# Kernel tuning notes

Measured on AMD Instinct MI355X. Metric: run time of the kernel, lower is better.

The kernel has to match this reference:

```python
import jax, jax.numpy as jnp
import numpy as np

N = 131072      # total nodes
B = 512         # number of graphs
F_DIM = 512     # in_channels
H = F_DIM // 2  # score_net hidden
RATIO = 0.5
MARGIN = 0.5
TOPK_LOSS_WEIGHT = 0.2


def setup_inputs() -> dict:
    key = jax.random.key(0)
    k1, k2, k3 = jax.random.split(key, 3)
    x = jax.random.normal(k1, (N, F_DIM), dtype=jnp.float32)
    # sorted segment ids: equal-sized graphs of N // B nodes
    batch = (jnp.arange(N) // (N // B)).astype(jnp.int32)
    W1 = jax.random.normal(k2, (F_DIM, H), dtype=jnp.float32) / np.sqrt(F_DIM).astype(np.float32)
    b1 = jnp.zeros((H,), dtype=jnp.float32)
    W2 = jax.random.normal(k3, (H, 1), dtype=jnp.float32) / np.sqrt(H).astype(np.float32)
    b2 = jnp.zeros((1,), dtype=jnp.float32)
    return {"x": x, "batch": batch, "W1": W1, "b1": b1, "W2": W2, "b2": b2}


def reference(x, batch, W1, b1, W2, b2):
    # scores = score_net(x).squeeze(-1)   [N]
    scores = (jax.nn.relu(x @ W1 + b1) @ W2 + b2)[:, 0]

    # per-graph node counts and k = max(1, int(ratio * n_i))
    counts = jax.ops.segment_sum(jnp.ones((N,), dtype=scores.dtype), batch, num_segments=B)
    k = jnp.maximum(1, jnp.floor(RATIO * counts).astype(jnp.int32))  # [B]

    # segmented top-k via lexsort: sort by (batch asc, score desc)
    order = jnp.lexsort((-scores, batch))          # [N] permutation
    b_sorted = batch[order]
    starts = jnp.cumsum(counts) - counts           # exclusive-cumsum segment starts
    rank = jnp.arange(N, dtype=counts.dtype) - starts[b_sorted]  # rank within graph (0 = highest score)
    sel_sorted = rank < k[b_sorted].astype(counts.dtype)
    selected_mask = jnp.zeros((N,), dtype=bool).at[order].set(sel_sorted)

    # global_add_pool over selected nodes
    m = selected_mask.astype(x.dtype)
    x_pooled = jax.ops.segment_sum(x * m[:, None], batch, num_segments=B)  # [B, F]

    # margin regularization loss per graph
    sel_cnt = jax.ops.segment_sum(m, batch, num_segments=B)
    sel_sum = jax.ops.segment_sum(scores * m, batch, num_segments=B)
    tot_sum = jax.ops.segment_sum(scores, batch, num_segments=B)
    uns_cnt = counts - sel_cnt
    sel_mean = sel_sum / jnp.maximum(sel_cnt, 1.0)
    uns_mean = (tot_sum - sel_sum) / jnp.maximum(uns_cnt, 1.0)
    per_graph = jnp.where(uns_cnt > 0, jax.nn.relu(MARGIN - (sel_mean - uns_mean)), 0.0)
    topk_loss = per_graph.sum() / B * TOPK_LOSS_WEIGHT

    return x_pooled, topk_loss, selected_mask
```

## Files before the change

kernel.cpp:

```cpp
#include <hip/hip_runtime.h>

#define BGRAPHS 512
#define FDIM    512
#define HDIM    256
#define NPG     256
#define KSEL    128
#define STAGES  32
#define BSTAGE_SHORTS 8192
#define BSTG    16384
#define A_ROW   24
#define A_PLANE (128 * A_ROW)

typedef __attribute__((ext_vector_type(8)))  _Float16 f16x8;
typedef __attribute__((ext_vector_type(8)))  short    s16x8;
typedef __attribute__((ext_vector_type(16))) float    f32x16;

__device__ __forceinline__ unsigned short f16_rne(float f, float* back) {
    _Float16 h = (_Float16)f;
    *back = (float)h;
    union { _Float16 h; unsigned short s; } cv; cv.h = h;
    return cv.s;
}

__global__ __launch_bounds__(256)
void split_w1_kernel(const float* __restrict__ W1, unsigned short* __restrict__ wsB,
                     float* __restrict__ out_loss)
{
    if (blockIdx.x == 0 && threadIdx.x == 0) out_loss[0] = 0.f;

    const int uid  = blockIdx.x * 256 + threadIdx.x;
    const int lane = uid & 63;
    int t = uid >> 6;
    const int nt = t & 7;  t >>= 3;
    const int p  = t & 1;  t >>= 1;
    const int s  = t;
    const int n  = nt * 32 + (lane & 31);
    const int k0 = s * 16 + (lane >> 5) * 8;

    s16x8 v;
    #pragma unroll
    for (int j = 0; j < 8; ++j) {
        float w = W1[(size_t)(k0 + j) * HDIM + n] * 1024.0f;
        float f1, f2;
        unsigned short h1 = f16_rne(w, &f1);
        unsigned short h2 = f16_rne(w - f1, &f2);
        v[j] = (short)(p ? h2 : h1);
    }
    *(s16x8*)(wsB + (size_t)uid * 8) = v;
}

__global__ __launch_bounds__(512, 4)
void gemm_kernel(const float* __restrict__ x,
                 const unsigned short* __restrict__ wsB,
                 const float* __restrict__ b1, const float* __restrict__ W2,
                 const float* __restrict__ b2,
                 float* __restrict__ scores_out)
{
    __shared__ __attribute__((aligned(16))) unsigned char smem[73728];

    const int bid  = blockIdx.x;
    const int g    = bid >> 1;
    const int rh   = bid & 1;
    const int tid  = threadIdx.x;
    const int lane = tid & 63;
    const int wv   = tid >> 6;
    const int wy   = wv & 1;
    const int wx   = wv >> 1;
    const int l31  = lane & 31;
    const int lh   = lane >> 5;

    const int arow  = tid >> 2;
    const int achk  = tid & 3;
    const float* aptr = x + ((size_t)(g * NPG + rh * 128 + arow)) * FDIM + achk * 4;

    f32x16 acc[2][2];
    #pragma unroll
    for (int a = 0; a < 2; ++a)
        #pragma unroll
        for (int b = 0; b < 2; ++b)
            #pragma unroll
            for (int rr = 0; rr < 16; ++rr) acc[a][b][rr] = 0.f;

    float4 pfA, pfB;

#define GLL_B(OFF, S1) do {                                                     \
    const unsigned short* _src = wsB + (size_t)(S1) * BSTAGE_SHORTS;            \
    unsigned short* _dst = (unsigned short*)(smem + (OFF));                     \
    _Pragma("unroll")                                                           \
    for (int _i = 0; _i < 2; ++_i) {                                            \
        const int _u = _i * 512 + tid;                                          \
        __builtin_amdgcn_global_load_lds(                                       \
            (const __attribute__((address_space(1))) unsigned int*)(_src + (size_t)_u * 8), \
            (__attribute__((address_space(3))) unsigned int*)(_dst + _u * 8),   \
            16, 0, 0);                                                          \
    } } while (0)

#define LOAD_PF(P,S2) do { P = *(const float4*)(aptr + (S2) * 16); } while (0)

#define CONVERT_A(P,BUF) do {                                                   \
    float _f[4] = {P.x, P.y, P.z, P.w};                                         \
    unsigned short _H[4], _M[4];                                                \
    _Pragma("unroll")                                                           \
    for (int _j = 0; _j < 4; ++_j) {                                            \
        float _b1v, _b2v;                                                       \
        float _xs = _f[_j] * 64.0f;                            \
        _H[_j] = f16_rne(_xs, &_b1v);                                           \
        _M[_j] = f16_rne(_xs - _b1v, &_b2v);                                    \
        (void)_b2v;                                                             \
    }                                                                           \
    unsigned short* _pl = (unsigned short*)(smem + 49152 + (BUF) * 12288)       \
                          + arow * A_ROW + achk * 4;                            \
    uint2 _uH, _uM;                                                             \
    _uH.x = (unsigned)_H[0] | ((unsigned)_H[1] << 16);                          \
    _uH.y = (unsigned)_H[2] | ((unsigned)_H[3] << 16);                          \
    _uM.x = (unsigned)_M[0] | ((unsigned)_M[1] << 16);                          \
    _uM.y = (unsigned)_M[2] | ((unsigned)_M[3] << 16);                          \
    *(uint2*)_pl = _uH;                                                         \
    *(uint2*)(_pl + A_PLANE) = _uM;                                             \
    } while (0)

#define COMPUTE(OFFB, ABUF) do {                                                \
    const f16x8* _bfp = (const f16x8*)(smem + (OFFB));                          \
    const unsigned short* _aB = (const unsigned short*)(smem + 49152 + (ABUF) * 12288); \
    const int _a0 = (wy * 64 + l31) * A_ROW + lh * 8;                           \
    f16x8 A0h = *(const f16x8*)(_aB + _a0);                                     \
    f16x8 A0m = *(const f16x8*)(_aB + A_PLANE + _a0);                           \
    f16x8 A1h = *(const f16x8*)(_aB + _a0 + 32 * A_ROW);                        \
    f16x8 A1m = *(const f16x8*)(_aB + A_PLANE + _a0 + 32 * A_ROW);              \
    const int _nn = wx * 2;                                                     \
    f16x8 Bh0 = _bfp[(0 * 8 + _nn + 0) * 64 + lane];                            \
    f16x8 Bh1 = _bfp[(0 * 8 + _nn + 1) * 64 + lane];                            \
    f16x8 Bm0 = _bfp[(1 * 8 + _nn + 0) * 64 + lane];                            \
    f16x8 Bm1 = _bfp[(1 * 8 + _nn + 1) * 64 + lane];                            \
    __builtin_amdgcn_s_setprio(1);                                              \
    acc[0][0] = __builtin_amdgcn_mfma_f32_32x32x16_f16(A0h, Bh0, acc[0][0], 0, 0, 0); \
    acc[0][1] = __builtin_amdgcn_mfma_f32_32x32x16_f16(A0h, Bh1, acc[0][1], 0, 0, 0); \
    acc[1][0] = __builtin_amdgcn_mfma_f32_32x32x16_f16(A1h, Bh0, acc[1][0], 0, 0, 0); \
    acc[1][1] = __builtin_amdgcn_mfma_f32_32x32x16_f16(A1h, Bh1, acc[1][1], 0, 0, 0); \
    acc[0][0] = __builtin_amdgcn_mfma_f32_32x32x16_f16(A0m, Bh0, acc[0][0], 0, 0, 0); \
    acc[0][1] = __builtin_amdgcn_mfma_f32_32x32x16_f16(A0m, Bh1, acc[0][1], 0, 0, 0); \
    acc[1][0] = __builtin_amdgcn_mfma_f32_32x32x16_f16(A1m, Bh0, acc[1][0], 0, 0, 0); \
    acc[1][1] = __builtin_amdgcn_mfma_f32_32x32x16_f16(A1m, Bh1, acc[1][1], 0, 0, 0); \
    acc[0][0] = __builtin_amdgcn_mfma_f32_32x32x16_f16(A0h, Bm0, acc[0][0], 0, 0, 0); \
    acc[0][1] = __builtin_amdgcn_mfma_f32_32x32x16_f16(A0h, Bm1, acc[0][1], 0, 0, 0); \
    acc[1][0] = __builtin_amdgcn_mfma_f32_32x32x16_f16(A1h, Bm0, acc[1][0], 0, 0, 0); \
    acc[1][1] = __builtin_amdgcn_mfma_f32_32x32x16_f16(A1h, Bm1, acc[1][1], 0, 0, 0); \
    __builtin_amdgcn_s_setprio(0);                                              \
    } while (0)

#define SYNC3 do {                                                              \
    asm volatile("s_waitcnt vmcnt(3) lgkmcnt(0)" ::: "memory");                 \
    __builtin_amdgcn_s_barrier();                                               \
    __builtin_amdgcn_sched_barrier(0); } while (0)
#define SYNC0 do {                                                              \
    asm volatile("s_waitcnt vmcnt(0) lgkmcnt(0)" ::: "memory");                 \
    __builtin_amdgcn_s_barrier();                                               \
    __builtin_amdgcn_sched_barrier(0); } while (0)

    LOAD_PF(pfA, 0);  GLL_B(0, 0);
    LOAD_PF(pfB, 1);  GLL_B(BSTG, 1);
    CONVERT_A(pfA, 0);
    SYNC3;

    int o0 = 0, o1 = BSTG, o2 = 2 * BSTG;
    for (int s = 0; s < 30; s += 2) {
        LOAD_PF(pfA, s + 2);  GLL_B(o2, s + 2);
        COMPUTE(o0, 0);
        CONVERT_A(pfB, 1);
        SYNC3;

        LOAD_PF(pfB, s + 3);  GLL_B(o0, s + 3);
        COMPUTE(o1, 1);
        CONVERT_A(pfA, 0);
        SYNC3;

        const int t = o0; o0 = o2; o2 = o1; o1 = t;
    }

    COMPUTE(o0, 0);
    CONVERT_A(pfB, 1);
    SYNC0;
    COMPUTE(o1, 1);

    float* scr = (float*)smem;

    float bb[2], ww[2];
    #pragma unroll
    for (int nt = 0; nt < 2; ++nt) {
        const int cc = wx * 64 + nt * 32 + l31;
        bb[nt] = b1[cc];
        ww[nt] = W2[cc];
    }
    const float unscale = 1.0f / 65536.0f;
    #pragma unroll
    for (int mt = 0; mt < 2; ++mt) {
        float pr[16];
        #pragma unroll
        for (int rr = 0; rr < 16; ++rr) pr[rr] = 0.f;
        #pragma unroll
        for (int nt = 0; nt < 2; ++nt)
            #pragma unroll
            for (int rr = 0; rr < 16; ++rr) {
                float h = fmaf(acc[mt][nt][rr], unscale, bb[nt]);
                h = h > 0.f ? h : 0.f;
                pr[rr] = fmaf(h, ww[nt], pr[rr]);
            }
        #pragma unroll
        for (int mask = 1; mask <= 16; mask <<= 1)
            #pragma unroll
            for (int rr = 0; rr < 16; ++rr)
                pr[rr] += __shfl_xor(pr[rr], mask);
        if (l31 == 0) {
            #pragma unroll
            for (int rr = 0; rr < 16; ++rr) {
                const int row = wy * 64 + mt * 32 + (rr & 3) + 8 * (rr >> 2) + 4 * lh;
                scr[wx * 128 + row] = pr[rr];
            }
        }
    }
    __syncthreads();

    if (tid < 128) {
        const float s = b2[0] + scr[tid] + scr[128 + tid] + scr[256 + tid] + scr[384 + tid];
        scores_out[(size_t)g * FDIM + rh * 128 + tid] = s;
    }

#undef GLL_B
#undef LOAD_PF
#undef CONVERT_A
#undef COMPUTE
#undef SYNC3
#undef SYNC0
}

__global__ __launch_bounds__(512)
void select_pool_kernel(const float* __restrict__ x,
                        float* __restrict__ pooled,
                        float* __restrict__ mask_out,
                        float* __restrict__ out_loss)
{
    __shared__ float sv[NPG];
    __shared__ int   selr[KSEL];
    __shared__ float redT[NPG];
    __shared__ float redS[NPG];

    const int g   = blockIdx.x;
    const int tid = threadIdx.x;

    float sc = 0.f;
    if (tid < NPG) {
        sc = pooled[(size_t)g * FDIM + tid];
        sv[tid] = sc;
    }
    __syncthreads();

    if (tid < NPG) {
        int rank = 0;
        for (int j = 0; j < NPG; ++j) {
            const float sj = sv[j];
            rank += (sj > sc || (sj == sc && j < tid)) ? 1 : 0;
        }
        const bool sel = rank < KSEL;
        mask_out[g * NPG + tid] = sel ? 1.0f : 0.0f;
        if (sel) selr[rank] = tid;
        redT[tid] = sc;
        redS[tid] = sel ? sc : 0.f;
    }
    __syncthreads();

    for (int off = 128; off > 0; off >>= 1) {
        if (tid < off) { redT[tid] += redT[tid + off]; redS[tid] += redS[tid + off]; }
        __syncthreads();
    }
    if (tid == 0) {
        const float tot = redT[0], ssum = redS[0];
        const float sel_mean = ssum * (1.0f / KSEL);
        const float uns_mean = (tot - ssum) * (1.0f / (NPG - KSEL));
        const float v = 0.5f - (sel_mean - uns_mean);
        if (v > 0.f) atomicAdd(out_loss, v * (0.2f / BGRAPHS));
    }

    const int col = tid;
    const float* __restrict__ xg = x + (size_t)g * NPG * FDIM;
    float a0 = 0.f, a1 = 0.f, a2 = 0.f, a3 = 0.f;
    float a4 = 0.f, a5 = 0.f, a6 = 0.f, a7 = 0.f;
    #pragma unroll 2
    for (int n = 0; n < KSEL; n += 8) {
        a0 += xg[(size_t)selr[n + 0] * FDIM + col];
        a1 += xg[(size_t)selr[n + 1] * FDIM + col];
        a2 += xg[(size_t)selr[n + 2] * FDIM + col];
        a3 += xg[(size_t)selr[n + 3] * FDIM + col];
        a4 += xg[(size_t)selr[n + 4] * FDIM + col];
        a5 += xg[(size_t)selr[n + 5] * FDIM + col];
        a6 += xg[(size_t)selr[n + 6] * FDIM + col];
        a7 += xg[(size_t)selr[n + 7] * FDIM + col];
    }
    pooled[(size_t)g * FDIM + col] = ((a0 + a1) + (a2 + a3)) + ((a4 + a5) + (a6 + a7));
}

extern "C" void kernel_launch(void* const* d_in, const int* in_sizes, int n_in,
                              void* d_out, int out_size, void* d_ws, size_t ws_size,
                              hipStream_t stream)
{
    const float* x  = (const float*)d_in[0];
    const float* W1 = (const float*)d_in[2];
    const float* b1 = (const float*)d_in[3];
    const float* W2 = (const float*)d_in[4];
    const float* b2 = (const float*)d_in[5];

    float* out    = (float*)d_out;
    float* pooled = out;
    float* loss   = out + BGRAPHS * FDIM;
    float* mask   = loss + 1;

    unsigned short* wsB = (unsigned short*)mask;

    split_w1_kernel<<<128, 256, 0, stream>>>(W1, wsB, loss);
    gemm_kernel<<<2 * BGRAPHS, 512, 0, stream>>>(x, wsB, b1, W2, b2, pooled);
    select_pool_kernel<<<BGRAPHS, 512, 0, stream>>>(x, pooled, mask, loss);
}
```

Measured before the change: 418.9 us.

## Load W1 fragments directly from global into registers instead of LDS staging

The GEMM kernel no longer stages the pre-split W1 fragments in shared memory with global_load_lds and a triple-buffered ring. Each wave now reads its B fragments straight from global memory (expected to hit in L2) into registers. Only the double-buffered A tile stays in LDS, which cuts shared memory from 72 KB to 24 KB per block and should allow more resident blocks per CU. It also drops the setprio hints and moves the A conversion ahead of the MFMAs. The cost is that the two waves sharing a column slice each fetch the same B data, doubling B reads from L2, and the B load latency now sits directly in front of the MFMAs.

```diff
diff --git a/kernel.cpp b/kernel.cpp
--- a/kernel.cpp
+++ b/kernel.cpp
@@ -5,9 +5,7 @@
 #define HDIM    256
 #define NPG     256
 #define KSEL    128
-#define STAGES  32
 #define BSTAGE_SHORTS 8192
-#define BSTG    16384
 #define A_ROW   24
 #define A_PLANE (128 * A_ROW)
 
@@ -56,7 +54,7 @@
                  const float* __restrict__ b2,
                  float* __restrict__ scores_out)
 {
-    __shared__ __attribute__((aligned(16))) unsigned char smem[73728];
+    __shared__ __attribute__((aligned(16))) unsigned char smem[24576];
 
     const int bid  = blockIdx.x;
     const int g    = bid >> 1;
@@ -68,6 +66,7 @@
     const int wx   = wv >> 1;
     const int l31  = lane & 31;
     const int lh   = lane >> 5;
+    const int nnB  = wx * 2;
 
     const int arow  = tid >> 2;
     const int achk  = tid & 3;
@@ -82,18 +81,6 @@
             for (int rr = 0; rr < 16; ++rr) acc[a][b][rr] = 0.f;
 
     float4 pfA, pfB;
-
-#define GLL_B(OFF, S1) do {                                                     \
-    const unsigned short* _src = wsB + (size_t)(S1) * BSTAGE_SHORTS;            \
-    unsigned short* _dst = (unsigned short*)(smem + (OFF));                     \
-    _Pragma("unroll")                                                           \
-    for (int _i = 0; _i < 2; ++_i) {                                            \
-        const int _u = _i * 512 + tid;                                          \
-        __builtin_amdgcn_global_load_lds(                                       \
-            (const __attribute__((address_space(1))) unsigned int*)(_src + (size_t)_u * 8), \
-            (__attribute__((address_space(3))) unsigned int*)(_dst + _u * 8),   \
-            16, 0, 0);                                                          \
-    } } while (0)
 
 #define LOAD_PF(P,S2) do { P = *(const float4*)(aptr + (S2) * 16); } while (0)
 
@@ -108,7 +95,7 @@
         _M[_j] = f16_rne(_xs - _b1v, &_b2v);                                    \
         (void)_b2v;                                                             \
     }                                                                           \
-    unsigned short* _pl = (unsigned short*)(smem + 49152 + (BUF) * 12288)       \
+    unsigned short* _pl = (unsigned short*)(smem) + (BUF) * (2 * A_PLANE)       \
                           + arow * A_ROW + achk * 4;                            \
     uint2 _uH, _uM;                                                             \
     _uH.x = (unsigned)_H[0] | ((unsigned)_H[1] << 16);                          \
@@ -119,20 +106,20 @@
     *(uint2*)(_pl + A_PLANE) = _uM;                                             \
     } while (0)
 
-#define COMPUTE(OFFB, ABUF) do {                                                \
-    const f16x8* _bfp = (const f16x8*)(smem + (OFFB));                          \
-    const unsigned short* _aB = (const unsigned short*)(smem + 49152 + (ABUF) * 12288); \
+#define BFRAG(S,P,J) \
+    (*(const f16x8*)(wsB + (size_t)((((S) * 2 + (P)) * 8 + nnB + (J)) * 64 + lane) * 8))
+
+#define COMPUTE(S, ABUF) do {                                                   \
+    f16x8 Bh0 = BFRAG(S, 0, 0);                                                 \
+    f16x8 Bh1 = BFRAG(S, 0, 1);                                                 \
+    f16x8 Bm0 = BFRAG(S, 1, 0);                                                 \
+    f16x8 Bm1 = BFRAG(S, 1, 1);                                                 \
+    const unsigned short* _aB = (const unsigned short*)(smem) + (ABUF) * (2 * A_PLANE); \
     const int _a0 = (wy * 64 + l31) * A_ROW + lh * 8;                           \
     f16x8 A0h = *(const f16x8*)(_aB + _a0);                                     \
     f16x8 A0m = *(const f16x8*)(_aB + A_PLANE + _a0);                           \
     f16x8 A1h = *(const f16x8*)(_aB + _a0 + 32 * A_ROW);                        \
     f16x8 A1m = *(const f16x8*)(_aB + A_PLANE + _a0 + 32 * A_ROW);              \
-    const int _nn = wx * 2;                                                     \
-    f16x8 Bh0 = _bfp[(0 * 8 + _nn + 0) * 64 + lane];                            \
-    f16x8 Bh1 = _bfp[(0 * 8 + _nn + 1) * 64 + lane];                            \
-    f16x8 Bm0 = _bfp[(1 * 8 + _nn + 0) * 64 + lane];                            \
-    f16x8 Bm1 = _bfp[(1 * 8 + _nn + 1) * 64 + lane];                            \
-    __builtin_amdgcn_s_setprio(1);                                              \
     acc[0][0] = __builtin_amdgcn_mfma_f32_32x32x16_f16(A0h, Bh0, acc[0][0], 0, 0, 0); \
     acc[0][1] = __builtin_amdgcn_mfma_f32_32x32x16_f16(A0h, Bh1, acc[0][1], 0, 0, 0); \
     acc[1][0] = __builtin_amdgcn_mfma_f32_32x32x16_f16(A1h, Bh0, acc[1][0], 0, 0, 0); \
@@ -145,42 +132,34 @@
     acc[0][1] = __builtin_amdgcn_mfma_f32_32x32x16_f16(A0h, Bm1, acc[0][1], 0, 0, 0); \
     acc[1][0] = __builtin_amdgcn_mfma_f32_32x32x16_f16(A1h, Bm0, acc[1][0], 0, 0, 0); \
     acc[1][1] = __builtin_amdgcn_mfma_f32_32x32x16_f16(A1h, Bm1, acc[1][1], 0, 0, 0); \
-    __builtin_amdgcn_s_setprio(0);                                              \
     } while (0)
 
-#define SYNC3 do {                                                              \
-    asm volatile("s_waitcnt vmcnt(3) lgkmcnt(0)" ::: "memory");                 \
+#define SYNCL do {                                                              \
+    asm volatile("s_waitcnt lgkmcnt(0)" ::: "memory");                          \
     __builtin_amdgcn_s_barrier();                                               \
     __builtin_amdgcn_sched_barrier(0); } while (0)
-#define SYNC0 do {                                                              \
-    asm volatile("s_waitcnt vmcnt(0) lgkmcnt(0)" ::: "memory");                 \
-    __builtin_amdgcn_s_barrier();                                               \
-    __builtin_amdgcn_sched_barrier(0); } while (0)
-
-    LOAD_PF(pfA, 0);  GLL_B(0, 0);
-    LOAD_PF(pfB, 1);  GLL_B(BSTG, 1);
+
+    LOAD_PF(pfA, 0);
     CONVERT_A(pfA, 0);
-    SYNC3;
-
-    int o0 = 0, o1 = BSTG, o2 = 2 * BSTG;
+    LOAD_PF(pfB, 1);
+    SYNCL;
+
     for (int s = 0; s < 30; s += 2) {
-        LOAD_PF(pfA, s + 2);  GLL_B(o2, s + 2);
-        COMPUTE(o0, 0);
+        LOAD_PF(pfA, s + 2);
         CONVERT_A(pfB, 1);
-        SYNC3;
-
-        LOAD_PF(pfB, s + 3);  GLL_B(o0, s + 3);
-        COMPUTE(o1, 1);
+        COMPUTE(s, 0);
+        SYNCL;
+
+        LOAD_PF(pfB, s + 3);
         CONVERT_A(pfA, 0);
-        SYNC3;
-
-        const int t = o0; o0 = o2; o2 = o1; o1 = t;
-    }
-
-    COMPUTE(o0, 0);
+        COMPUTE(s + 1, 1);
+        SYNCL;
+    }
+
     CONVERT_A(pfB, 1);
-    SYNC0;
-    COMPUTE(o1, 1);
+    COMPUTE(30, 0);
+    SYNCL;
+    COMPUTE(31, 1);
 
     float* scr = (float*)smem;
 
@@ -225,12 +204,11 @@
         scores_out[(size_t)g * FDIM + rh * 128 + tid] = s;
     }
 
-#undef GLL_B
 #undef LOAD_PF
 #undef CONVERT_A
+#undef BFRAG
 #undef COMPUTE
-#undef SYNC3
-#undef SYNC0
+#undef SYNCL
 }
 
 __global__ __launch_bounds__(512)
```

Measured after the change: 427.3 us. No clear change (+2.0%).
